# Kernel optimization log

Hardware: AMD Instinct MI355X
Metric: run time of the kernel (lower is better)

## Reference

```python
import jax, jax.numpy as jnp
import numpy as np

B, C, H, W = 512, 3, 32, 32
N = 50000
D = C * H * W  # 3072


def setup_inputs() -> dict:
    key = jax.random.key(0)
    k1, k2, k3 = jax.random.split(key, 3)
    x = jax.random.normal(k1, (B, C, H, W), dtype=jnp.float32)
    # per-sample noise levels, strictly positive
    sigma = jax.random.uniform(k2, (B,), dtype=jnp.float32, minval=0.5, maxval=2.0)
    # reference dataset, normalized images in [-1, 1], flattened to (N, D)
    y = jax.random.uniform(k3, (N, D), dtype=jnp.float32, minval=-1.0, maxval=1.0)
    return {"x": x, "sigma": sigma, "y": y}


def reference(x, sigma, y):
    Bb, Cc, Hh, Ww = x.shape
    xf = x.astype(jnp.float32).reshape(Bb, Cc * Hh * Ww)          # (B, D)
    s = sigma.astype(jnp.float32).reshape(-1, 1)                  # (B, 1)
    # squared euclidean distance via the GEMM expansion (matches cdist(p=2)**2)
    x2 = jnp.sum(xf * xf, axis=1, keepdims=True)                  # (B, 1)
    y2 = jnp.sum(y * y, axis=1)[None, :]                          # (1, N)
    d2 = jnp.maximum(x2 + y2 - 2.0 * (xf @ y.T), 0.0)             # (B, N)
    logits = -d2 / (2.0 * s * s)                                  # (B, N)
    prob = jax.nn.softmax(logits, axis=1)                         # (B, N)
    denoised = prob @ y                                           # (B, D)
    return denoised.reshape(Bb, Cc, Hh, Ww)
```

## Files before the change

### kernel.cpp

```cpp
#include <hip/hip_runtime.h>


typedef __attribute__((ext_vector_type(4))) float f32x4;
typedef __attribute__((ext_vector_type(4))) int i32x4;
typedef __attribute__((ext_vector_type(4))) char c8x4;
typedef __attribute__((ext_vector_type(16))) char c8x16;
typedef __attribute__((ext_vector_type(4))) unsigned short u16x4;
typedef __attribute__((ext_vector_type(8))) unsigned short u16x8;
typedef __attribute__((ext_vector_type(8))) __bf16 bf16x8;

#define NREAL 50000
#define NP    50176
#define DD    3072
#define BB    512

#define WAIT0  asm volatile("s_waitcnt vmcnt(0)" ::: "memory")
#define VM2    asm volatile("s_waitcnt vmcnt(2)" ::: "memory")
#define LGKM0  asm volatile("s_waitcnt lgkmcnt(0)" ::: "memory")
#define BAR    __builtin_amdgcn_s_barrier()
#define SCHED0 __builtin_amdgcn_sched_barrier(0)

#define SX (6.0f / 127.0f)
#define SY (1.0f / 127.0f)

__device__ __forceinline__ unsigned short f32_bf16_rne(float f) {
  unsigned int u = __float_as_uint(f);
  unsigned int r = 0x7FFFu + ((u >> 16) & 1u);
  return (unsigned short)((u + r) >> 16);
}
__device__ __forceinline__ void gload16(const void* g, void* l) {
  __builtin_amdgcn_global_load_lds(
      (const __attribute__((address_space(1))) void*)g,
      (__attribute__((address_space(3))) void*)l, 16, 0, 0);
}
__device__ __forceinline__ bf16x8 ldsldb(const unsigned short* p) {
  return __builtin_bit_cast(bf16x8, *(const u16x8*)p);
}
__device__ __forceinline__ i32x4 ldsld4(const char* p) {
  return *(const i32x4*)p;
}
__device__ __forceinline__ char q8(float f, float sc) {
  float an = rintf(f * sc);
  an = fminf(127.f, fmaxf(-127.f, an));
  return (char)(int)an;
}

__global__ __launch_bounds__(256) void zero_kernel(f32x4* p) {
  p[(size_t)blockIdx.x * 256 + threadIdx.x] = (f32x4){0.f, 0.f, 0.f, 0.f};
}

__global__ __launch_bounds__(256) void init_kernel(int* rowmin, float* rowsum) {
  const int i = blockIdx.x * 256 + threadIdx.x;
  if (i < BB) { rowmin[i] = 0x7F800000; rowsum[i] = 0.f; }
}

__global__ __launch_bounds__(256) void prep_x_kernel(
    const float* __restrict__ x, const float* __restrict__ sigma,
    char* __restrict__ ax, char* __restrict__ bx,
    float* __restrict__ x2, float* __restrict__ inv2s2) {
  const int b = blockIdx.x, t = threadIdx.x;
  const f32x4* xr = (const f32x4*)(x + (size_t)b * DD);
  float ssq = 0.f;
#pragma unroll
  for (int i = 0; i < 3; ++i) {
    const int idx = i * 256 + t;
    f32x4 v = xr[idx];
    c8x4 a, bb;
#pragma unroll
    for (int j = 0; j < 4; ++j) {
      float f = v[j];
      ssq += f * f;
      char av = q8(f, 127.0f / 6.0f);
      a[j] = av;
      float r = f - (float)(int)av * SX;
      bb[j] = q8(r, 254.0f * 127.0f / 6.0f);
    }
    *(c8x4*)(ax + (size_t)b * DD + idx * 4) = a;
    *(c8x4*)(bx + (size_t)b * DD + idx * 4) = bb;
  }
  __shared__ float red[4];
#pragma unroll
  for (int off = 32; off > 0; off >>= 1) ssq += __shfl_xor(ssq, off);
  if ((t & 63) == 0) red[t >> 6] = ssq;
  __syncthreads();
  if (t == 0) {
    x2[b] = red[0] + red[1] + red[2] + red[3];
    float s = sigma[b];
    inv2s2[b] = 1.0f / (2.0f * s * s);
  }
}

__global__ __launch_bounds__(256) void quant_y_kernel(
    const float* __restrict__ y, char* __restrict__ ay, char* __restrict__ by,
    float* __restrict__ y2) {
  const int n = blockIdx.x, t = threadIdx.x;
  if (n >= NREAL) {
    c8x4 z = {0, 0, 0, 0};
#pragma unroll
    for (int i = 0; i < 3; ++i) {
      const int idx = i * 256 + t;
      *(c8x4*)(ay + (size_t)n * DD + idx * 4) = z;
      *(c8x4*)(by + (size_t)n * DD + idx * 4) = z;
    }
    if (t == 0) y2[n] = 0.f;
    return;
  }
  const f32x4* yr = (const f32x4*)(y + (size_t)n * DD);
  float ssq = 0.f;
#pragma unroll
  for (int i = 0; i < 3; ++i) {
    const int idx = i * 256 + t;
    f32x4 v = yr[idx];
    c8x4 a, bb;
#pragma unroll
    for (int j = 0; j < 4; ++j) {
      float f = v[j];
      ssq += f * f;
      char av = q8(f, 127.0f);
      a[j] = av;
      float r2 = f - (float)(int)av * SY;
      bb[j] = q8(r2, 254.0f * 127.0f);
    }
    *(c8x4*)(ay + (size_t)n * DD + idx * 4) = a;
    *(c8x4*)(by + (size_t)n * DD + idx * 4) = bb;
  }
  __shared__ float red[4];
#pragma unroll
  for (int off = 32; off > 0; off >>= 1) ssq += __shfl_xor(ssq, off);
  if ((t & 63) == 0) red[t >> 6] = ssq;
  __syncthreads();
  if (t == 0) y2[n] = red[0] + red[1] + red[2] + red[3];
}

__global__ __launch_bounds__(256) void tr_y_kernel(
    const char* __restrict__ ay, const char* __restrict__ by,
    unsigned short* __restrict__ yT) {
  const int bn = blockIdx.x % 784, bd = blockIdx.x / 784;
  const int n0 = bn * 64, d0 = bd * 64;
  __shared__ unsigned short T[64][66];
  const int t = threadIdx.x;
  const int r = t >> 2, cc = (t & 3) * 16;
  c8x16 a = *(const c8x16*)(ay + (size_t)(n0 + r) * DD + d0 + cc);
  c8x16 b = *(const c8x16*)(by + (size_t)(n0 + r) * DD + d0 + cc);
#pragma unroll
  for (int j = 0; j < 16; ++j) {
    float f = (float)((int)a[j] * 254 + (int)b[j]) * (SY / 254.0f);
    T[r][cc + j] = f32_bf16_rne(f);
  }
  __syncthreads();
  const int dr = t >> 2;
#pragma unroll
  for (int k = 0; k < 2; ++k) {
    const int nb = (t & 3) * 16 + k * 8;
    u16x8 o;
#pragma unroll
    for (int j = 0; j < 8; ++j) o[j] = T[nb + j][dr];
    *(u16x8*)(yT + (size_t)(d0 + dr) * NP + n0 + nb) = o;
  }
}

__global__ __launch_bounds__(256, 2) void qk_kernel(
    const char* __restrict__ ay, const char* __restrict__ by,
    const char* __restrict__ ax, const char* __restrict__ bx,
    const float* __restrict__ x2, const float* __restrict__ inv2s2,
    const float* __restrict__ y2, float* __restrict__ S, int* __restrict__ rowmin) {
  const int orig = blockIdx.x;
  const int virt = (orig & 7) * 196 + (orig >> 3);
  const int mt = virt & 3, nt = virt >> 2;
  const int m0 = mt * 128, n0 = nt * 128;
  const int t = threadIdx.x, lane = t & 63, w = t >> 6;
  const int wm = w >> 1, wn = w & 1;
  const int l15 = lane & 15;
  const int cs = ((lane >> 4) ^ ((l15 >> 1) & 3)) * 16;

  __shared__ __align__(16) char L[32768];

  i32x4 acc1[4][4] = {};
  i32x4 acc2[4][4] = {};

  const int srow = t >> 2;
  const int sc = ((t & 3) ^ ((t >> 3) & 3)) * 16;
  const int sdst = t * 16;

  const char* pax0 = ax + (size_t)(m0 + srow) * DD + sc;
  const char* pax1 = ax + (size_t)(m0 + srow + 64) * DD + sc;
  const char* pbx0 = bx + (size_t)(m0 + srow) * DD + sc;
  const char* pbx1 = bx + (size_t)(m0 + srow + 64) * DD + sc;
  const char* pay0 = ay + (size_t)(n0 + srow) * DD + sc;
  const char* pay1 = ay + (size_t)(n0 + srow + 64) * DD + sc;
  const char* pby0 = by + (size_t)(n0 + srow) * DD + sc;
  const char* pby1 = by + (size_t)(n0 + srow + 64) * DD + sc;

  auto STAGE = [&]() {
    gload16(pax0, L + sdst);
    gload16(pax1, L + 4096 + sdst);
    gload16(pbx0, L + 8192 + sdst);
    gload16(pbx1, L + 12288 + sdst);
    gload16(pay0, L + 16384 + sdst);
    gload16(pay1, L + 20480 + sdst);
    gload16(pby0, L + 24576 + sdst);
    gload16(pby1, L + 28672 + sdst);
    pax0 += 64; pax1 += 64; pbx0 += 64; pbx1 += 64;
    pay0 += 64; pay1 += 64; pby0 += 64; pby1 += 64;
  };
  auto COMPUTE = [&]() {
    i32x4 axf[4], bxf[4], ayf[4], byf[4];
#pragma unroll
    for (int nf = 0; nf < 4; ++nf) {
      const int row = wn * 64 + nf * 16 + l15;
      ayf[nf] = ldsld4(L + 16384 + row * 64 + cs);
      byf[nf] = ldsld4(L + 24576 + row * 64 + cs);
    }
#pragma unroll
    for (int mf = 0; mf < 4; ++mf) {
      const int row = wm * 64 + mf * 16 + l15;
      axf[mf] = ldsld4(L + row * 64 + cs);
      bxf[mf] = ldsld4(L + 8192 + row * 64 + cs);
    }
    __builtin_amdgcn_s_setprio(1);
#pragma unroll
    for (int mf = 0; mf < 4; ++mf)
#pragma unroll
      for (int nf = 0; nf < 4; ++nf) {
        acc1[mf][nf] = __builtin_amdgcn_mfma_i32_16x16x64_i8(axf[mf], ayf[nf], acc1[mf][nf], 0, 0, 0);
        acc2[mf][nf] = __builtin_amdgcn_mfma_i32_16x16x64_i8(axf[mf], byf[nf], acc2[mf][nf], 0, 0, 0);
        acc2[mf][nf] = __builtin_amdgcn_mfma_i32_16x16x64_i8(bxf[mf], ayf[nf], acc2[mf][nf], 0, 0, 0);
      }
    __builtin_amdgcn_s_setprio(0);
  };

  STAGE();
  for (int k = 0; k < 48; ++k) {
    __syncthreads();
    COMPUTE();
    __syncthreads();
    if (k < 47) STAGE();
  }

  const float C1 = 6.0f / 16129.0f;
  const float C2 = C1 / 254.0f;
  float rmv[4][4];
#pragma unroll
  for (int mf = 0; mf < 4; ++mf)
#pragma unroll
    for (int i = 0; i < 4; ++i) rmv[mf][i] = 3.0e38f;

#pragma unroll
  for (int nf = 0; nf < 4; ++nf) {
    const int col = n0 + wn * 64 + nf * 16 + l15;
    const bool ok = (col < NREAL);
    const float yy = ok ? y2[col] : 0.f;
#pragma unroll
    for (int mf = 0; mf < 4; ++mf) {
#pragma unroll
      for (int i = 0; i < 4; ++i) {
        const int row = m0 + wm * 64 + mf * 16 + ((lane >> 4) * 4) + i;
        float v = 3.0e38f;
        if (ok) {
          float dot = C1 * (float)acc1[mf][nf][i] + C2 * (float)acc2[mf][nf][i];
          float d2 = fmaxf(x2[row] + yy - 2.0f * dot, 0.0f);
          v = d2 * inv2s2[row];
          rmv[mf][i] = fminf(rmv[mf][i], v);
        }
        S[(size_t)row * NP + col] = v;
      }
    }
  }
#pragma unroll
  for (int mf = 0; mf < 4; ++mf)
#pragma unroll
    for (int i = 0; i < 4; ++i) {
      float v = rmv[mf][i];
#pragma unroll
      for (int o = 1; o < 16; o <<= 1) v = fminf(v, __shfl_xor(v, o));
      rmv[mf][i] = v;
    }
  if (l15 == 0) {
#pragma unroll
    for (int mf = 0; mf < 4; ++mf)
#pragma unroll
      for (int i = 0; i < 4; ++i) {
        const int row = m0 + wm * 64 + mf * 16 + ((lane >> 4) * 4) + i;
        atomicMin(rowmin + row, __float_as_int(rmv[mf][i]));
      }
  }
}

__global__ __launch_bounds__(256) void softmax_kernel(
    const float* __restrict__ S, const int* __restrict__ rowmin,
    unsigned short* __restrict__ P, float* __restrict__ rowsum) {
  const int bid = blockIdx.x;
  const int b = bid / 7, c = bid % 7;
  const int t = threadIdx.x;
  const f32x4* row = (const f32x4*)(S + (size_t)b * NP);
  const float rm = __int_as_float(rowmin[b]);
  unsigned short* pr = P + (size_t)b * NP;
  float sum = 0.f;
  const int base = c * 1792;
#pragma unroll
  for (int i = 0; i < 7; ++i) {
    const int e = base + i * 256 + t;
    f32x4 v = row[e];
    float e0 = __expf(rm - v[0]), e1 = __expf(rm - v[1]);
    float e2 = __expf(rm - v[2]), e3 = __expf(rm - v[3]);
    sum += e0 + e1 + e2 + e3;
    u16x4 o;
    o[0] = f32_bf16_rne(e0); o[1] = f32_bf16_rne(e1);
    o[2] = f32_bf16_rne(e2); o[3] = f32_bf16_rne(e3);
    *(u16x4*)(pr + (size_t)e * 4) = o;
  }
#pragma unroll
  for (int off = 32; off > 0; off >>= 1) sum += __shfl_xor(sum, off);
  __shared__ float red[4];
  if ((t & 63) == 0) red[t >> 6] = sum;
  __syncthreads();
  if (t == 0) atomicAdd(rowsum + b, red[0] + red[1] + red[2] + red[3]);
}

__global__ __launch_bounds__(512, 2) void pv_kernel(
    const unsigned short* __restrict__ yT, const unsigned short* __restrict__ P,
    const float* __restrict__ rowsum, float* __restrict__ out) {
  const int orig = blockIdx.x;
  const int virt = (orig & 7) * 96 + (orig >> 3);
  const int sp = virt / 24;
  const int r24 = virt % 24;
  const int dt = r24 >> 1, mt = r24 & 1;
  const int m0 = mt * 256, d0 = dt * 256;
  const int k0t = sp * 24 + (sp < 16 ? sp : 16);
  const int NT = 24 + (sp < 16 ? 1 : 0);

  const int t = threadIdx.x;
  const int lane = t & 63, w = t >> 6;
  const int wm = w >> 2, wn = w & 3;
  const int l15 = lane & 15;
  const int h3 = (l15 >> 1) & 7;
  const int cs0 = ((lane >> 4) ^ h3) * 8;
  const int cs1 = ((4 + (lane >> 4)) ^ h3) * 8;

  __shared__ __align__(16) unsigned short L[2][2][16384];

  f32x4 acc[8][4] = {};

  const int srow8 = t >> 3;
  const int sc = ((t & 7) ^ ((t >> 4) & 7)) * 8;
  const int sdst = t * 8;

  const size_t kbeg = (size_t)k0t * 64;
  const unsigned short* pA[4];
  pA[0] = P + (size_t)(m0 + srow8) * NP + kbeg + sc;
  pA[1] = P + (size_t)(m0 + srow8 + 128) * NP + kbeg + sc;
  pA[2] = P + (size_t)(m0 + srow8 + 64) * NP + kbeg + sc;
  pA[3] = P + (size_t)(m0 + srow8 + 192) * NP + kbeg + sc;
  const unsigned short* pB[4];
#pragma unroll
  for (int r = 0; r < 4; ++r)
    pB[r] = yT + (size_t)(d0 + srow8 + r * 64) * NP + kbeg + sc;

  auto SB01 = [&](int b) {
    gload16(pB[0], &L[b][1][sdst]); gload16(pB[1], &L[b][1][sdst + 4096]);
    pB[0] += 64; pB[1] += 64;
  };
  auto SB23 = [&](int b) {
    gload16(pB[2], &L[b][1][sdst + 8192]); gload16(pB[3], &L[b][1][sdst + 12288]);
    pB[2] += 64; pB[3] += 64;
  };
  auto SA01 = [&](int b) {
    gload16(pA[0], &L[b][0][sdst]); gload16(pA[1], &L[b][0][sdst + 4096]);
    pA[0] += 64; pA[1] += 64;
  };
  auto SA23 = [&](int b) {
    gload16(pA[2], &L[b][0][sdst + 8192]); gload16(pA[3], &L[b][0][sdst + 12288]);
    pA[2] += 64; pA[3] += 64;
  };

  bf16x8 a[4], bv[4];
  auto RA = [&](int b, int mh, int cs) {
#pragma unroll
    for (int m4 = 0; m4 < 4; ++m4)
      a[m4] = ldsldb(&L[b][0][(mh * 128 + wm * 64 + m4 * 16 + l15) * 64 + cs]);
  };
  auto RB = [&](int b, int cs) {
#pragma unroll
    for (int nf = 0; nf < 4; ++nf)
      bv[nf] = ldsldb(&L[b][1][(wn * 64 + nf * 16 + l15) * 64 + cs]);
  };
  auto MF = [&](int mh) {
    __builtin_amdgcn_s_setprio(1);
#pragma unroll
    for (int m4 = 0; m4 < 4; ++m4)
#pragma unroll
      for (int nf = 0; nf < 4; ++nf)
        acc[mh * 4 + m4][nf] = __builtin_amdgcn_mfma_f32_16x16x32_bf16(
            a[m4], bv[nf], acc[mh * 4 + m4][nf], 0, 0, 0);
    __builtin_amdgcn_s_setprio(0);
  };

  SB01(0); SB23(0); SA01(0); SA23(0);
  WAIT0; BAR;

  for (int k = 0; k < NT - 1; ++k) {
    const int b = k & 1, nb = b ^ 1;
    RB(b, cs0); RA(b, 0, cs0);
    SB01(nb);
    BAR; LGKM0; SCHED0;
    MF(0);
    VM2;
    BAR;
    RA(b, 1, cs0);
    SB23(nb);
    BAR; LGKM0; SCHED0;
    MF(1);
    BAR;
    RB(b, cs1); RA(b, 0, cs1);
    SA01(nb);
    BAR; LGKM0; SCHED0;
    MF(0);
    BAR;
    RA(b, 1, cs1);
    SA23(nb);
    BAR; LGKM0; SCHED0;
    MF(1);
    VM2;
    BAR;
  }
  {
    const int b = (NT - 1) & 1;
    RB(b, cs0); RA(b, 0, cs0);
    BAR; LGKM0; SCHED0;
    MF(0);
    WAIT0;
    BAR;
    RA(b, 1, cs0);
    LGKM0; SCHED0;
    MF(1);
    RB(b, cs1); RA(b, 0, cs1);
    LGKM0; SCHED0;
    MF(0);
    RA(b, 1, cs1);
    LGKM0; SCHED0;
    MF(1);
  }

#pragma unroll
  for (int mi = 0; mi < 8; ++mi)
#pragma unroll
    for (int i = 0; i < 4; ++i) {
      const int row = m0 + wm * 128 + mi * 16 + ((lane >> 4) * 4) + i;
      const float scale = 1.0f / rowsum[row];
#pragma unroll
      for (int nf = 0; nf < 4; ++nf) {
        const int col = d0 + wn * 64 + nf * 16 + l15;
        unsafeAtomicAdd(out + (size_t)row * DD + col, acc[mi][nf][i] * scale);
      }
    }
}

extern "C" void kernel_launch(void* const* d_in, const int* in_sizes, int n_in,
                              void* d_out, int out_size, void* d_ws, size_t ws_size,
                              hipStream_t stream) {
  const float* x = (const float*)d_in[0];
  const float* sigma = (const float*)d_in[1];
  const float* y = (const float*)d_in[2];
  float* out = (float*)d_out;
  char* ws = (char*)d_ws;

  size_t off = 0;
  float* S = (float*)(ws + off);                      off += (size_t)BB * NP * 4;
  char* ay = (char*)(ws + off);                       off += (size_t)NP * DD;
  char* by = (char*)(ws + off);                       off += (size_t)NP * DD;
  unsigned short* P = (unsigned short*)by;
  char* ax = (char*)(ws + off);                       off += (size_t)BB * DD;
  char* bx = (char*)(ws + off);                       off += (size_t)BB * DD;
  float* y2 = (float*)(ws + off);                     off += (size_t)NP * 4;
  float* x2 = (float*)(ws + off);                     off += 512 * 4;
  float* inv2s2 = (float*)(ws + off);                 off += 512 * 4;
  float* rowsum = (float*)(ws + off);                 off += 512 * 4;
  int* rowmin = (int*)(ws + off);                     off += 512 * 4;
  unsigned short* yT = (unsigned short*)(ws + off);   off += (size_t)DD * NP * 2;
  off += 65536;
  if (ws_size < off) return;

  zero_kernel<<<dim3(1536), dim3(256), 0, stream>>>((f32x4*)out);
  init_kernel<<<dim3(2), dim3(256), 0, stream>>>(rowmin, rowsum);
  prep_x_kernel<<<dim3(512), dim3(256), 0, stream>>>(x, sigma, ax, bx, x2, inv2s2);
  quant_y_kernel<<<dim3(NP), dim3(256), 0, stream>>>(y, ay, by, y2);
  tr_y_kernel<<<dim3(784 * 48), dim3(256), 0, stream>>>(ay, by, yT);
  qk_kernel<<<dim3(1568), dim3(256), 0, stream>>>(ay, by, ax, bx, x2, inv2s2, y2, S, rowmin);
  softmax_kernel<<<dim3(512 * 7), dim3(256), 0, stream>>>(S, rowmin, P, rowsum);
  pv_kernel<<<dim3(768), dim3(512), 0, stream>>>(yT, P, rowsum, out);
}
```

Measured before the change: 913.8 us.

## Double-buffer LDS tiles in qk_kernel with partial vmcnt waits

Doubles the shared-memory staging buffer in the int8 QK GEMM kernel and prefetches the next K-slice while the current one is computed. Explicit vmcnt(8) waits replace the full syncthreads drain, so global-to-LDS loads for the next tile overlap the MFMA work. LDS use per block doubles to 64KB, which may lower occupancy under launch_bounds(256,2).

```diff
diff --git a/kernel.cpp b/kernel.cpp
--- a/kernel.cpp
+++ b/kernel.cpp
@@ -16,6 +16,7 @@
 
 #define WAIT0  asm volatile("s_waitcnt vmcnt(0)" ::: "memory")
 #define VM2    asm volatile("s_waitcnt vmcnt(2)" ::: "memory")
+#define VM8    asm volatile("s_waitcnt vmcnt(8)" ::: "memory")
 #define LGKM0  asm volatile("s_waitcnt lgkmcnt(0)" ::: "memory")
 #define BAR    __builtin_amdgcn_s_barrier()
 #define SCHED0 __builtin_amdgcn_sched_barrier(0)
@@ -173,7 +174,7 @@
   const int l15 = lane & 15;
   const int cs = ((lane >> 4) ^ ((l15 >> 1) & 3)) * 16;
 
-  __shared__ __align__(16) char L[32768];
+  __shared__ __align__(16) char L[2][32768];
 
   i32x4 acc1[4][4] = {};
   i32x4 acc2[4][4] = {};
@@ -191,31 +192,33 @@
   const char* pby0 = by + (size_t)(n0 + srow) * DD + sc;
   const char* pby1 = by + (size_t)(n0 + srow + 64) * DD + sc;
 
-  auto STAGE = [&]() {
-    gload16(pax0, L + sdst);
-    gload16(pax1, L + 4096 + sdst);
-    gload16(pbx0, L + 8192 + sdst);
-    gload16(pbx1, L + 12288 + sdst);
-    gload16(pay0, L + 16384 + sdst);
-    gload16(pay1, L + 20480 + sdst);
-    gload16(pby0, L + 24576 + sdst);
-    gload16(pby1, L + 28672 + sdst);
+  auto STAGE = [&](int buf) {
+    char* B = L[buf];
+    gload16(pax0, B + sdst);
+    gload16(pax1, B + 4096 + sdst);
+    gload16(pbx0, B + 8192 + sdst);
+    gload16(pbx1, B + 12288 + sdst);
+    gload16(pay0, B + 16384 + sdst);
+    gload16(pay1, B + 20480 + sdst);
+    gload16(pby0, B + 24576 + sdst);
+    gload16(pby1, B + 28672 + sdst);
     pax0 += 64; pax1 += 64; pbx0 += 64; pbx1 += 64;
     pay0 += 64; pay1 += 64; pby0 += 64; pby1 += 64;
   };
-  auto COMPUTE = [&]() {
+  auto COMPUTE = [&](int buf) {
+    const char* B = L[buf];
     i32x4 axf[4], bxf[4], ayf[4], byf[4];
 #pragma unroll
     for (int nf = 0; nf < 4; ++nf) {
       const int row = wn * 64 + nf * 16 + l15;
-      ayf[nf] = ldsld4(L + 16384 + row * 64 + cs);
-      byf[nf] = ldsld4(L + 24576 + row * 64 + cs);
+      ayf[nf] = ldsld4(B + 16384 + row * 64 + cs);
+      byf[nf] = ldsld4(B + 24576 + row * 64 + cs);
     }
 #pragma unroll
     for (int mf = 0; mf < 4; ++mf) {
       const int row = wm * 64 + mf * 16 + l15;
-      axf[mf] = ldsld4(L + row * 64 + cs);
-      bxf[mf] = ldsld4(L + 8192 + row * 64 + cs);
+      axf[mf] = ldsld4(B + row * 64 + cs);
+      bxf[mf] = ldsld4(B + 8192 + row * 64 + cs);
     }
     __builtin_amdgcn_s_setprio(1);
 #pragma unroll
@@ -229,12 +232,14 @@
     __builtin_amdgcn_s_setprio(0);
   };
 
-  STAGE();
+  STAGE(0);
+  STAGE(1);
   for (int k = 0; k < 48; ++k) {
-    __syncthreads();
-    COMPUTE();
-    __syncthreads();
-    if (k < 47) STAGE();
+    if (k < 47) { VM8; } else { WAIT0; }
+    BAR;
+    COMPUTE(k & 1);
+    BAR;
+    if (k < 46) STAGE(k & 1);
   }
 
   const float C1 = 6.0f / 16129.0f;
```

Result: faster. 871.8 us (-4.6%).
